# Optimization experiments

Hardware: AMD Instinct MI355X
Metric: run time of the kernel (lower is better)

Reference implementation:

```python
import jax, jax.numpy as jnp
import numpy as np

N = 16384
D_IN = 128
LAYERS = [128, 128, 128, 10]
LATENT = [64, 64]


def _linear_params(key, fan_in, fan_out):
    k1, k2 = jax.random.split(key)
    bound = 1.0 / np.sqrt(fan_in)
    w = jax.random.uniform(k1, (fan_in, fan_out), minval=-bound, maxval=bound, dtype=jnp.float32)
    b = jax.random.uniform(k2, (fan_out,), minval=-bound, maxval=bound, dtype=jnp.float32)
    return w, b


def setup_inputs() -> dict:
    key = jax.random.key(0)
    ks = jax.random.split(key, 8)
    feat_matrix = jax.random.normal(ks[0], (N, D_IN), dtype=jnp.float32)
    gl_w0, gl_b0 = _linear_params(ks[1], LAYERS[0], LATENT[0])
    gnn_w0, gnn_b0 = _linear_params(ks[2], LAYERS[0], LAYERS[1])
    gl_w1, gl_b1 = _linear_params(ks[3], LAYERS[1], LATENT[1])
    gnn_w1, gnn_b1 = _linear_params(ks[4], LAYERS[1], LAYERS[2])
    out_w, out_b = _linear_params(ks[5], LAYERS[2], LAYERS[3])
    return {
        "feat_matrix": feat_matrix,
        "gl_w0": gl_w0, "gl_b0": gl_b0,
        "gl_w1": gl_w1, "gl_b1": gl_b1,
        "gnn_w0": gnn_w0, "gnn_b0": gnn_b0,
        "gnn_w1": gnn_w1, "gnn_b1": gnn_b1,
        "out_w": out_w, "out_b": out_b,
        "temp": jnp.float32(0.1),
        "theta": jnp.float32(0.1),
        "adj_matrix": jnp.zeros((N, N), dtype=jnp.float32),
        "get_item_index": jax.random.randint(ks[6], (1024,), 0, N, dtype=jnp.int32),
        "set_index": jax.random.randint(ks[7], (1024,), 0, N, dtype=jnp.int32),
        "val_index": jax.random.randint(jax.random.fold_in(key, 9), (1024,), 0, N, dtype=jnp.int32),
        "mask_matrix": jnp.zeros((N,), dtype=bool),
    }


def _layer(x, gl_w, gl_b, gnn_w, gnn_b, temp, theta):
    # graph-learning projection
    g = jax.nn.relu(x @ gl_w + gl_b)                     # [N, L]
    # pairwise squared L2 distances (utils.l2_mat)
    sq = jnp.sum(g * g, axis=-1)                         # [N]
    dist = sq[:, None] + sq[None, :] - 2.0 * (g @ g.T)   # [N, N]
    t = 1.0 + temp
    th = 5.0 + theta
    adj = jax.nn.sigmoid(t * (-dist) + th)               # [N, N]
    # diag(rowsum).inverse() @ adj @ gnn(x) == row-normalized message passing
    msg = adj @ (x @ gnn_w + gnn_b)                      # [N, H]
    return msg / jnp.sum(adj, axis=-1, keepdims=True)


def reference(feat_matrix, gl_w0, gl_b0, gl_w1, gl_b1,
              gnn_w0, gnn_b0, gnn_w1, gnn_b1,
              out_w, out_b, temp, theta,
              adj_matrix, get_item_index, set_index, val_index, mask_matrix):
    x = feat_matrix
    x = jax.nn.relu(_layer(x, gl_w0, gl_b0, gnn_w0, gnn_b0, temp, theta))
    x = _layer(x, gl_w1, gl_b1, gnn_w1, gnn_b1, temp, theta)  # last gnn layer: no relu
    x = x @ out_w + out_b
    return jax.nn.softmax(x, axis=-1)
```

## Files before the change

### kernel.cpp

```cpp
#include <hip/hip_runtime.h>

#define NN 16384
#define DL 64
#define HD 128
#define BMW 32
#define BM 128
#define BN 64
#define JS 8
#define JCH (NN / JS)
#define NITER (JCH / BN)

typedef _Float16 v8h __attribute__((ext_vector_type(8)));
typedef __fp16 v2fp16 __attribute__((ext_vector_type(2)));
typedef float v16f __attribute__((ext_vector_type(16)));
typedef unsigned short ushort_t;
typedef unsigned int uint32;

__device__ __forceinline__ float bf2f(ushort_t v) {
  return __uint_as_float(((uint32)v) << 16);
}
__device__ __forceinline__ ushort_t f2bf(float f) {
  uint32 u = __float_as_uint(f);
  return (ushort_t)((u + 0x7FFFu + ((u >> 16) & 1u)) >> 16);
}
__device__ __forceinline__ uint32 pack2h(float a, float b) {
  union { v2fp16 h; uint32 u; } p;
  p.h = __builtin_amdgcn_cvt_pkrtz(a, b);
  return p.u;
}
__device__ __forceinline__ void gld16(void* lds, const void* gp) {
  __builtin_amdgcn_global_load_lds(
      (const __attribute__((address_space(1))) uint32*)gp,
      (__attribute__((address_space(3))) uint32*)lds, 16, 0, 0);
}

__global__ void detect_k(const void* __restrict__ feat,
                         const void* __restrict__ temp,
                         const void* __restrict__ theta,
                         float* __restrict__ consts) {
  const int l = threadIdx.x;
  const ushort_t* u = (const ushort_t*)feat;
  float v0 = fabsf(bf2f(u[2 * l]));
  float v1 = fabsf(bf2f(u[2 * l + 1]));
  int ok = ((v0 > 1e-4f && v0 < 16.0f) ? 1 : 0) +
           ((v1 > 1e-4f && v1 < 16.0f) ? 1 : 0);
#pragma unroll
  for (int off = 1; off < 64; off <<= 1) ok += __shfl_xor(ok, off, 64);
  if (l == 0) {
    int isbf = (ok >= 100) ? 1 : 0;
    float tv, th;
    if (isbf) {
      tv = bf2f(((const ushort_t*)temp)[0]);
      th = bf2f(((const ushort_t*)theta)[0]);
    } else {
      tv = ((const float*)temp)[0];
      th = ((const float*)theta)[0];
    }
    consts[0] = (float)isbf;
    consts[1] = 1.0f + tv;
    consts[2] = 5.0f + th;
    consts[3] = 2.0f * (1.0f + tv) * 1.44269504088896341f;
  }
}

template <int L0>
__global__ __launch_bounds__(256) void prep_k(
    const void* __restrict__ xb, const float* __restrict__ msgp,
    const float* __restrict__ denp, const void* __restrict__ glw,
    const void* __restrict__ glb, const void* __restrict__ gnw,
    const void* __restrict__ gnb, const float* __restrict__ cst,
    _Float16* __restrict__ g, _Float16* __restrict__ hT,
    float* __restrict__ crow) {
  __shared__ float xr[4][128];
  const int w = threadIdx.x >> 6, l = threadIdx.x & 63;
  const int row = blockIdx.x * 4 + w;
  const int isbf = (cst[0] != 0.0f);
  float x0, x1;
  if (L0) {
    if (isbf) {
      const ushort_t* p = (const ushort_t*)xb;
      x0 = bf2f(p[row * 128 + 2 * l]);
      x1 = bf2f(p[row * 128 + 2 * l + 1]);
    } else {
      const float* p = (const float*)xb;
      x0 = p[row * 128 + 2 * l];
      x1 = p[row * 128 + 2 * l + 1];
    }
  } else {
    float m0 = 0.0f, m1 = 0.0f, d = 0.0f;
#pragma unroll
    for (int js = 0; js < JS; ++js) {
      const float* mp = msgp + (size_t)js * NN * HD + (size_t)row * HD;
      m0 += mp[2 * l];
      m1 += mp[2 * l + 1];
      d += denp[js * NN + row];
    }
    float rd = __builtin_amdgcn_rcpf(fmaxf(d, 1e-10f));
    x0 = fmaxf(m0 * rd, 0.0f);
    x1 = fmaxf(m1 * rd, 0.0f);
  }
  xr[w][2 * l] = x0;
  xr[w][2 * l + 1] = x1;
  __syncthreads();
  float ag = 0.0f, a0 = 0.0f, a1 = 0.0f;
  float bg, b0, b1;
  if (isbf) {
    const ushort_t* Wg = (const ushort_t*)glw;
    const ushort_t* Wn = (const ushort_t*)gnw;
#pragma unroll 8
    for (int k = 0; k < 128; ++k) {
      float xk = xr[w][k];
      ag = fmaf(xk, bf2f(Wg[k * 64 + l]), ag);
      a0 = fmaf(xk, bf2f(Wn[k * 128 + l]), a0);
      a1 = fmaf(xk, bf2f(Wn[k * 128 + 64 + l]), a1);
    }
    bg = bf2f(((const ushort_t*)glb)[l]);
    b0 = bf2f(((const ushort_t*)gnb)[l]);
    b1 = bf2f(((const ushort_t*)gnb)[64 + l]);
  } else {
    const float* Wg = (const float*)glw;
    const float* Wn = (const float*)gnw;
#pragma unroll 8
    for (int k = 0; k < 128; ++k) {
      float xk = xr[w][k];
      ag = fmaf(xk, Wg[k * 64 + l], ag);
      a0 = fmaf(xk, Wn[k * 128 + l], a0);
      a1 = fmaf(xk, Wn[k * 128 + 64 + l], a1);
    }
    bg = ((const float*)glb)[l];
    b0 = ((const float*)gnb)[l];
    b1 = ((const float*)gnb)[64 + l];
  }
  const float t = cst[1];
  const float th = cst[2];
  float gv = fmaxf(ag + bg, 0.0f);
  _Float16 gq = (_Float16)gv;
  g[(size_t)row * DL + l] = gq;
  float gf = (float)gq;
  float sq = gf * gf;
#pragma unroll
  for (int off = 1; off < 64; off <<= 1) sq += __shfl_xor(sq, off, 64);
  if (l == 0) crow[row] = (0.5f * th - t * sq) * 1.44269504088896341f;
  hT[(size_t)l * NN + row] = (_Float16)(a0 + b0);
  hT[(size_t)(l + 64) * NN + row] = (_Float16)(a1 + b1);
}

__global__ __launch_bounds__(256, 2) void attn_main(
    const _Float16* __restrict__ g, const _Float16* __restrict__ hT,
    const float* __restrict__ crow, const float* __restrict__ cst,
    float* __restrict__ msgp, float* __restrict__ denp) {
  __shared__ __align__(16) short SM[2 * 12288];

  const int tid = threadIdx.x;
  const int w = tid >> 6;
  const int l = tid & 63;
  const int ln = l & 31;
  const int hb = l >> 5;
  const int iw = blockIdx.x * BM + w * BMW;
  const int jb = blockIdx.y * JCH;
  const float s2 = cst[3];

  v8h Bi[4];
#pragma unroll
  for (int kf = 0; kf < 4; ++kf)
    Bi[kf] = *(const v8h*)(g + (size_t)(iw + ln) * DL + kf * 16 + hb * 8);

  const float ci = crow[iw + ln];

  v16f o[4];
#pragma unroll
  for (int mp = 0; mp < 4; ++mp)
#pragma unroll
    for (int r = 0; r < 16; ++r) o[mp][r] = 0.0f;

  float dp = 0.0f;

  auto stage = [&](int p, int j0) {
    char* Gb = (char*)(SM + p * 12288);
    char* Hb = (char*)(SM + p * 12288 + 4096);
#pragma unroll
    for (int oo = 0; oo < 2; ++oo) {
      int c = oo * 256 + tid;
      int jj = c >> 3, pc = c & 7;
      int kc = pc ^ (jj & 7);
      gld16(Gb + (oo * 256 + w * 64) * 16, g + (size_t)(j0 + jj) * DL + kc * 8);
    }
#pragma unroll
    for (int oo = 0; oo < 4; ++oo) {
      int c = oo * 256 + tid;
      int hc = c >> 3, pc = c & 7;
      int jc = pc ^ (hc & 7);
      gld16(Hb + (oo * 256 + w * 64) * 16, hT + (size_t)hc * NN + j0 + jc * 8);
    }
  };

  stage(0, jb);

#pragma unroll 1
  for (int itr = 0; itr < NITER; ++itr) {
    const int j0 = jb + itr * BN;
    const int p = itr & 1;
    __syncthreads();
    if (itr + 1 < NITER) stage(p ^ 1, j0 + BN);
    _Float16* Gs = (_Float16*)(SM + p * 12288);
    _Float16* Hs = (_Float16*)(SM + p * 12288 + 4096);

#pragma unroll
    for (int jt = 0; jt < 2; ++jt) {
      float cj[16];
#pragma unroll
      for (int q2 = 0; q2 < 4; ++q2) {
        float4 f4 = *(const float4*)(crow + j0 + jt * 32 + q2 * 8 + 4 * hb);
        cj[q2 * 4 + 0] = f4.x;
        cj[q2 * 4 + 1] = f4.y;
        cj[q2 * 4 + 2] = f4.z;
        cj[q2 * 4 + 3] = f4.w;
      }
      v16f sv;
#pragma unroll
      for (int r = 0; r < 16; ++r) sv[r] = 0.0f;
#pragma unroll
      for (int kf = 0; kf < 4; ++kf) {
        int row = jt * 32 + ln;
        int kc = kf * 2 + hb;
        v8h a = *(const v8h*)(Gs + row * 64 + ((kc ^ (row & 7)) * 8));
        sv = __builtin_amdgcn_mfma_f32_32x32x16_f16(a, Bi[kf], sv, 0, 0, 0);
      }
      float pv[16];
      float dps = 0.0f;
#pragma unroll
      for (int r = 0; r < 16; ++r) {
        float arg = fmaf(s2, sv[r], ci) + cj[r];
        float e = __builtin_amdgcn_exp2f(-arg);
        float adj = 256.0f * __builtin_amdgcn_rcpf(1.0f + e);
        dps += adj;
        pv[r] = adj;
      }
      dp += dps;
#pragma unroll
      for (int kq = 0; kq < 2; ++kq) {
        int q = kq * 8;
        uint32 lo0 = pack2h(pv[q + 0], pv[q + 1]);
        uint32 lo1 = pack2h(pv[q + 2], pv[q + 3]);
        uint32 hi0 = pack2h(pv[q + 4], pv[q + 5]);
        uint32 hi1 = pack2h(pv[q + 6], pv[q + 7]);
        uint32 sl0 = (uint32)__shfl_xor((int)lo0, 32, 64);
        uint32 sl1 = (uint32)__shfl_xor((int)lo1, 32, 64);
        uint32 sh0 = (uint32)__shfl_xor((int)hi0, 32, 64);
        uint32 sh1 = (uint32)__shfl_xor((int)hi1, 32, 64);
        union { uint32 u[4]; v8h v; } b;
        b.u[0] = hb ? sh0 : lo0;
        b.u[1] = hb ? sh1 : lo1;
        b.u[2] = hb ? hi0 : sl0;
        b.u[3] = hb ? hi1 : sl1;
        int kc = (jt * 2 + kq) * 2 + hb;
#pragma unroll
        for (int mp = 0; mp < 4; ++mp) {
          int hc = mp * 32 + ln;
          v8h Ah = *(const v8h*)(Hs + hc * 64 + ((kc ^ (hc & 7)) * 8));
          o[mp] = __builtin_amdgcn_mfma_f32_32x32x16_f16(Ah, b.v, o[mp], 0, 0, 0);
        }
      }
    }
  }

  dp += __shfl_xor(dp, 32, 64);
  if (hb == 0) denp[blockIdx.y * NN + iw + ln] = dp;
  __syncthreads();
  float* Tw = ((float*)SM) + w * (32 * 33);
  float* mout = msgp + (size_t)blockIdx.y * NN * HD;
#pragma unroll
  for (int mp = 0; mp < 4; ++mp) {
#pragma unroll
    for (int r = 0; r < 16; ++r) {
      int hl = (r & 3) + 8 * (r >> 2) + 4 * hb;
      Tw[ln * 33 + hl] = o[mp][r];
    }
#pragma unroll
    for (int rr = 0; rr < 16; ++rr) {
      int il = rr * 2 + hb;
      mout[(size_t)(iw + il) * HD + mp * 32 + ln] = Tw[il * 33 + ln];
    }
  }
}

__global__ __launch_bounds__(256) void final_k(
    const float* __restrict__ msgp, const float* __restrict__ denp,
    const void* __restrict__ ow, const void* __restrict__ ob,
    const float* __restrict__ cst, void* __restrict__ out) {
  __shared__ float Ws[1280];
  const int isbf = (cst[0] != 0.0f);
  if (isbf) {
    for (int i = threadIdx.x; i < 1280; i += 256) Ws[i] = bf2f(((const ushort_t*)ow)[i]);
  } else {
    for (int i = threadIdx.x; i < 1280; i += 256) Ws[i] = ((const float*)ow)[i];
  }
  __syncthreads();
  const int l16 = threadIdx.x & 15, grp = threadIdx.x >> 4;
  const int row = blockIdx.x * 16 + grp;
  float d = 0.0f;
#pragma unroll
  for (int js = 0; js < JS; ++js) d += denp[js * NN + row];
  const float rd = __builtin_amdgcn_rcpf(fmaxf(d, 1e-10f));
  float acc[10];
#pragma unroll
  for (int c = 0; c < 10; ++c) acc[c] = 0.0f;
#pragma unroll
  for (int kk = 0; kk < 8; ++kk) {
    int k = kk * 16 + l16;
    float m = 0.0f;
#pragma unroll
    for (int js = 0; js < JS; ++js)
      m += msgp[(size_t)js * NN * HD + (size_t)row * HD + k];
    float xv = m * rd;
    xv = fminf(fmaxf(xv, -1e6f), 1e6f);
#pragma unroll
    for (int c = 0; c < 10; ++c) acc[c] = fmaf(xv, Ws[k * 10 + c], acc[c]);
  }
  float bias[10];
  if (isbf) {
#pragma unroll
    for (int c = 0; c < 10; ++c) bias[c] = bf2f(((const ushort_t*)ob)[c]);
  } else {
#pragma unroll
    for (int c = 0; c < 10; ++c) bias[c] = ((const float*)ob)[c];
  }
#pragma unroll
  for (int c = 0; c < 10; ++c) {
#pragma unroll
    for (int off = 1; off < 16; off <<= 1) acc[c] += __shfl_xor(acc[c], off, 64);
    acc[c] += bias[c];
  }
  float m = acc[0];
#pragma unroll
  for (int c = 1; c < 10; ++c) m = fmaxf(m, acc[c]);
  float s = 0.0f, e[10];
#pragma unroll
  for (int c = 0; c < 10; ++c) {
    e[c] = __builtin_amdgcn_exp2f((acc[c] - m) * 1.44269504088896341f);
    s += e[c];
  }
  float rs = __builtin_amdgcn_rcpf(s);
  float mine = e[0];
#pragma unroll
  for (int c = 1; c < 10; ++c) mine = (l16 == c) ? e[c] : mine;
  if (l16 < 10) {
    float v = mine * rs;
    if (isbf) ((ushort_t*)out)[(size_t)row * 10 + l16] = f2bf(v);
    else ((float*)out)[(size_t)row * 10 + l16] = v;
  }
}

extern "C" void kernel_launch(void* const* d_in, const int* in_sizes, int n_in,
                              void* d_out, int out_size, void* d_ws,
                              size_t ws_size, hipStream_t stream) {
  const void* feat = d_in[0];
  const void* glw0 = d_in[1];
  const void* glb0 = d_in[2];
  const void* glw1 = d_in[3];
  const void* glb1 = d_in[4];
  const void* gnw0 = d_in[5];
  const void* gnb0 = d_in[6];
  const void* gnw1 = d_in[7];
  const void* gnb1 = d_in[8];
  const void* ow = d_in[9];
  const void* obv = d_in[10];
  const void* temp = d_in[11];
  const void* thet = d_in[12];

  char* ws = (char*)d_ws;
  _Float16* g = (_Float16*)ws;
  _Float16* hT = (_Float16*)(ws + (size_t)(2u << 20));
  float* crow = (float*)(ws + (size_t)(6u << 20));
  float* cst = (float*)(ws + (size_t)(6u << 20) + (1u << 16));
  float* msgp = (float*)(ws + (size_t)(7u << 20));
  float* denp = (float*)(ws + (size_t)(71u << 20));

  dim3 b256(256);
  detect_k<<<dim3(1), dim3(64), 0, stream>>>(feat, temp, thet, cst);
  prep_k<1><<<dim3(NN / 4), b256, 0, stream>>>(feat, nullptr, nullptr, glw0,
                                               glb0, gnw0, gnb0, cst, g, hT,
                                               crow);
  attn_main<<<dim3(NN / BM, JS), b256, 0, stream>>>(g, hT, crow, cst, msgp,
                                                    denp);
  prep_k<0><<<dim3(NN / 4), b256, 0, stream>>>(nullptr, msgp, denp, glw1, glb1,
                                               gnw1, gnb1, cst, g, hT, crow);
  attn_main<<<dim3(NN / BM, JS), b256, 0, stream>>>(g, hT, crow, cst, msgp,
                                                    denp);
  final_k<<<dim3(NN / 16), b256, 0, stream>>>(msgp, denp, ow, obv, cst, d_out);
}
```

Measured before the change: 1.582 ms.

## Process two 32-row i tiles per wave to reuse staged G/H fragments

Each wave now handles 64 query rows instead of 32, so every LDS read of the key-side G fragment and the H fragment feeds two MFMAs instead of one, and the block covers 256 rows. This halves LDS traffic and staging per unit of work and halves the number of blocks along i. The sigmoid is rewritten as rcp(exp2(arg) + 1/256) with the constants folded in, which drops a negate and a multiply per element. In exchange the accumulator registers double (128 floats of o), which may hurt occupancy under launch_bounds(256,2) or cause spills, and fewer blocks may leave the GPU under-filled.

```diff
diff --git a/kernel.cpp b/kernel.cpp
--- a/kernel.cpp
+++ b/kernel.cpp
@@ -3,8 +3,8 @@
 #define NN 16384
 #define DL 64
 #define HD 128
-#define BMW 32
-#define BM 128
+#define BMW 64
+#define BM 256
 #define BN 64
 #define JS 8
 #define JCH (NN / JS)
@@ -158,22 +158,28 @@
   const int hb = l >> 5;
   const int iw = blockIdx.x * BM + w * BMW;
   const int jb = blockIdx.y * JCH;
-  const float s2 = cst[3];
-
-  v8h Bi[4];
-#pragma unroll
-  for (int kf = 0; kf < 4; ++kf)
-    Bi[kf] = *(const v8h*)(g + (size_t)(iw + ln) * DL + kf * 16 + hb * 8);
-
-  const float ci = crow[iw + ln];
-
-  v16f o[4];
+  const float negs2 = -cst[3];
+
+  v8h Bi[2][4];
+#pragma unroll
+  for (int it = 0; it < 2; ++it)
+#pragma unroll
+    for (int kf = 0; kf < 4; ++kf)
+      Bi[it][kf] =
+          *(const v8h*)(g + (size_t)(iw + it * 32 + ln) * DL + kf * 16 + hb * 8);
+
+  const float cin0 = -crow[iw + ln] - 8.0f;
+  const float cin1 = -crow[iw + 32 + ln] - 8.0f;
+
+  v16f o[4][2];
 #pragma unroll
   for (int mp = 0; mp < 4; ++mp)
 #pragma unroll
-    for (int r = 0; r < 16; ++r) o[mp][r] = 0.0f;
-
-  float dp = 0.0f;
+    for (int it = 0; it < 2; ++it)
+#pragma unroll
+      for (int r = 0; r < 16; ++r) o[mp][it][r] = 0.0f;
+
+  float dp0 = 0.0f, dp1 = 0.0f;
 
   auto stage = [&](int p, int j0) {
     char* Gb = (char*)(SM + p * 12288);
@@ -216,72 +222,95 @@
         cj[q2 * 4 + 2] = f4.z;
         cj[q2 * 4 + 3] = f4.w;
       }
-      v16f sv;
-#pragma unroll
-      for (int r = 0; r < 16; ++r) sv[r] = 0.0f;
+      v16f sv[2];
+#pragma unroll
+      for (int r = 0; r < 16; ++r) {
+        sv[0][r] = 0.0f;
+        sv[1][r] = 0.0f;
+      }
 #pragma unroll
       for (int kf = 0; kf < 4; ++kf) {
         int row = jt * 32 + ln;
         int kc = kf * 2 + hb;
         v8h a = *(const v8h*)(Gs + row * 64 + ((kc ^ (row & 7)) * 8));
-        sv = __builtin_amdgcn_mfma_f32_32x32x16_f16(a, Bi[kf], sv, 0, 0, 0);
-      }
-      float pv[16];
-      float dps = 0.0f;
-#pragma unroll
-      for (int r = 0; r < 16; ++r) {
-        float arg = fmaf(s2, sv[r], ci) + cj[r];
-        float e = __builtin_amdgcn_exp2f(-arg);
-        float adj = 256.0f * __builtin_amdgcn_rcpf(1.0f + e);
-        dps += adj;
-        pv[r] = adj;
-      }
-      dp += dps;
+        sv[0] = __builtin_amdgcn_mfma_f32_32x32x16_f16(a, Bi[0][kf], sv[0], 0, 0, 0);
+        sv[1] = __builtin_amdgcn_mfma_f32_32x32x16_f16(a, Bi[1][kf], sv[1], 0, 0, 0);
+      }
+      uint32 Bf[2][2][4];
+#pragma unroll
+      for (int it = 0; it < 2; ++it) {
+        float pv[16];
+        float dps = 0.0f;
+        float cin = it ? cin1 : cin0;
+#pragma unroll
+        for (int r = 0; r < 16; ++r) {
+          float ap = fmaf(negs2, sv[it][r], cin) - cj[r];
+          float e2 = __builtin_amdgcn_exp2f(ap);
+          float adj = __builtin_amdgcn_rcpf(e2 + 0.00390625f);
+          dps += adj;
+          pv[r] = adj;
+        }
+        if (it == 0) dp0 += dps; else dp1 += dps;
+#pragma unroll
+        for (int kq = 0; kq < 2; ++kq) {
+          int q = kq * 8;
+          uint32 lo0 = pack2h(pv[q + 0], pv[q + 1]);
+          uint32 lo1 = pack2h(pv[q + 2], pv[q + 3]);
+          uint32 hi0 = pack2h(pv[q + 4], pv[q + 5]);
+          uint32 hi1 = pack2h(pv[q + 6], pv[q + 7]);
+          uint32 sl0 = (uint32)__shfl_xor((int)lo0, 32, 64);
+          uint32 sl1 = (uint32)__shfl_xor((int)lo1, 32, 64);
+          uint32 sh0 = (uint32)__shfl_xor((int)hi0, 32, 64);
+          uint32 sh1 = (uint32)__shfl_xor((int)hi1, 32, 64);
+          Bf[it][kq][0] = hb ? sh0 : lo0;
+          Bf[it][kq][1] = hb ? sh1 : lo1;
+          Bf[it][kq][2] = hb ? hi0 : sl0;
+          Bf[it][kq][3] = hb ? hi1 : sl1;
+        }
+      }
 #pragma unroll
       for (int kq = 0; kq < 2; ++kq) {
-        int q = kq * 8;
-        uint32 lo0 = pack2h(pv[q + 0], pv[q + 1]);
-        uint32 lo1 = pack2h(pv[q + 2], pv[q + 3]);
-        uint32 hi0 = pack2h(pv[q + 4], pv[q + 5]);
-        uint32 hi1 = pack2h(pv[q + 6], pv[q + 7]);
-        uint32 sl0 = (uint32)__shfl_xor((int)lo0, 32, 64);
-        uint32 sl1 = (uint32)__shfl_xor((int)lo1, 32, 64);
-        uint32 sh0 = (uint32)__shfl_xor((int)hi0, 32, 64);
-        uint32 sh1 = (uint32)__shfl_xor((int)hi1, 32, 64);
-        union { uint32 u[4]; v8h v; } b;
-        b.u[0] = hb ? sh0 : lo0;
-        b.u[1] = hb ? sh1 : lo1;
-        b.u[2] = hb ? hi0 : sl0;
-        b.u[3] = hb ? hi1 : sl1;
+        union { uint32 u[4]; v8h v; } b0, b1;
+        b0.u[0] = Bf[0][kq][0]; b0.u[1] = Bf[0][kq][1];
+        b0.u[2] = Bf[0][kq][2]; b0.u[3] = Bf[0][kq][3];
+        b1.u[0] = Bf[1][kq][0]; b1.u[1] = Bf[1][kq][1];
+        b1.u[2] = Bf[1][kq][2]; b1.u[3] = Bf[1][kq][3];
         int kc = (jt * 2 + kq) * 2 + hb;
 #pragma unroll
         for (int mp = 0; mp < 4; ++mp) {
           int hc = mp * 32 + ln;
           v8h Ah = *(const v8h*)(Hs + hc * 64 + ((kc ^ (hc & 7)) * 8));
-          o[mp] = __builtin_amdgcn_mfma_f32_32x32x16_f16(Ah, b.v, o[mp], 0, 0, 0);
+          o[mp][0] = __builtin_amdgcn_mfma_f32_32x32x16_f16(Ah, b0.v, o[mp][0], 0, 0, 0);
+          o[mp][1] = __builtin_amdgcn_mfma_f32_32x32x16_f16(Ah, b1.v, o[mp][1], 0, 0, 0);
         }
       }
     }
   }
 
-  dp += __shfl_xor(dp, 32, 64);
-  if (hb == 0) denp[blockIdx.y * NN + iw + ln] = dp;
+  dp0 += __shfl_xor(dp0, 32, 64);
+  dp1 += __shfl_xor(dp1, 32, 64);
+  if (hb == 0) {
+    denp[blockIdx.y * NN + iw + ln] = dp0;
+    denp[blockIdx.y * NN + iw + 32 + ln] = dp1;
+  }
   __syncthreads();
   float* Tw = ((float*)SM) + w * (32 * 33);
   float* mout = msgp + (size_t)blockIdx.y * NN * HD;
 #pragma unroll
-  for (int mp = 0; mp < 4; ++mp) {
-#pragma unroll
-    for (int r = 0; r < 16; ++r) {
-      int hl = (r & 3) + 8 * (r >> 2) + 4 * hb;
-      Tw[ln * 33 + hl] = o[mp][r];
-    }
-#pragma unroll
-    for (int rr = 0; rr < 16; ++rr) {
-      int il = rr * 2 + hb;
-      mout[(size_t)(iw + il) * HD + mp * 32 + ln] = Tw[il * 33 + ln];
-    }
-  }
+  for (int mp = 0; mp < 4; ++mp)
+#pragma unroll
+    for (int it = 0; it < 2; ++it) {
+#pragma unroll
+      for (int r = 0; r < 16; ++r) {
+        int hl = (r & 3) + 8 * (r >> 2) + 4 * hb;
+        Tw[ln * 33 + hl] = o[mp][it][r];
+      }
+#pragma unroll
+      for (int rr = 0; rr < 16; ++rr) {
+        int il = rr * 2 + hb;
+        mout[(size_t)(iw + it * 32 + il) * HD + mp * 32 + ln] = Tw[il * 33 + ln];
+      }
+    }
 }
 
 __global__ __launch_bounds__(256) void final_k(
```

Measured after the change: 1.671 ms. 1.06x slower.
